# Kernel optimization log

Measured on AMD Instinct MI355X. Metric: run time of the kernel, lower is better.

Reference implementation:

```python
import jax, jax.numpy as jnp
import numpy as np

D_MODEL = 1024
N_HEAD = 16
D_HEAD = D_MODEL // N_HEAD
B, S = 4, 2048


def setup_inputs() -> dict:
    key = jax.random.key(0)
    ks = jax.random.split(key, 10)
    def xavier(k, shape):
        fan_in, fan_out = shape[1], shape[0]
        limit = np.sqrt(6.0 / (fan_in + fan_out))
        return jax.random.uniform(k, shape, jnp.float32, -limit, limit)
    x = jax.random.normal(ks[0], (B, S, D_MODEL), jnp.float32)
    mask = jnp.tril(jnp.ones((S, S), jnp.int32))[None, None]  # causal [1,1,S,S]
    return {
        "x": x,
        "Wq": xavier(ks[1], (D_MODEL, D_MODEL)), "bq": jnp.zeros((D_MODEL,), jnp.float32),
        "Wk": xavier(ks[2], (D_MODEL, D_MODEL)), "bk": jnp.zeros((D_MODEL,), jnp.float32),
        "Wv": xavier(ks[3], (D_MODEL, D_MODEL)), "bv": jnp.zeros((D_MODEL,), jnp.float32),
        "Wo": xavier(ks[4], (D_MODEL, D_MODEL)), "bo": jnp.zeros((D_MODEL,), jnp.float32),
        "mask": mask,
    }


def reference(x, Wq, bq, Wk, bk, Wv, bv, Wo, bo, mask):
    b, s, d = x.shape
    # Linear layers use y = x @ W.T + b (torch convention)
    def proj(W, bias):
        y = jnp.einsum('bsd,ed->bse', x, W) + bias
        return y.reshape(b, s, N_HEAD, D_HEAD).transpose(0, 2, 1, 3)  # [B,H,S,Dh]
    q = proj(Wq, bq)
    k = proj(Wk, bk)
    v = proj(Wv, bv)
    scores = jnp.einsum('bhqd,bhkd->bhqk', q, k) / jnp.sqrt(jnp.float32(D_HEAD))
    scores = jnp.where(mask == 0, jnp.float32(-1e9), scores)
    attn = jax.nn.softmax(scores, axis=-1)  # dropout is identity at eval
    context = jnp.einsum('bhqk,bhkd->bhqd', attn, v)
    context = context.transpose(0, 2, 1, 3).reshape(b, s, d)
    return jnp.einsum('bsd,ed->bse', context, Wo) + bo
```

## Files before the change

### kernel.cpp

```cpp
#include <hip/hip_runtime.h>
#include <stdint.h>

#define D_MODEL 1024
#define NHEAD   16
#define DHEAD   64
#define BATCH   4
#define SEQ     2048
#define MTOT    (BATCH*SEQ)

typedef __attribute__((ext_vector_type(4)))  float f32x4;
typedef __attribute__((ext_vector_type(8)))  short bf16x8;

typedef __attribute__((address_space(3))) uint32_t lds_u32;
typedef const __attribute__((address_space(1))) uint32_t glb_u32;

__device__ static inline void gload_lds16(const void* g, void* l) {
    __builtin_amdgcn_global_load_lds((glb_u32*)g, (lds_u32*)l, 16, 0, 0);
}

__device__ static inline ushort f2bf(float f) {
    uint32_t u = __builtin_bit_cast(uint32_t, f);
    u += 0x7fffu + ((u >> 16) & 1u);
    return (ushort)(u >> 16);
}

__device__ static inline float exp2_fast(float x) {
    float r; asm("v_exp_f32 %0, %1" : "=v"(r) : "v"(x)); return r;
}
__device__ static inline uint32_t cvt_pk_bf16(float a, float b) {
    uint32_t r;
    asm("v_cvt_pk_bf16_f32 %0, %1, %2" : "=v"(r) : "v"(a), "v"(b));
    return r;
}

__global__ __launch_bounds__(256) void convert_kernel(
    const float4* __restrict__ x,
    const float4* __restrict__ wq, const float4* __restrict__ wk,
    const float4* __restrict__ wv, const float4* __restrict__ wo,
    ushort4* __restrict__ xb, ushort4* __restrict__ wb)
{
    const int NX4 = (MTOT * D_MODEL) / 4;
    const int NW4 = (D_MODEL * D_MODEL) / 4;
    const int TOT = NX4 + 4 * NW4;
    for (int i = blockIdx.x * blockDim.x + threadIdx.x; i < TOT;
         i += gridDim.x * blockDim.x) {
        float4 v; ushort4* dst;
        if (i < NX4) { v = x[i]; dst = &xb[i]; }
        else {
            int j = i - NX4;
            int w = j >> 18;
            int r = j & (NW4 - 1);
            const float4* s = (w == 0) ? wq : (w == 1) ? wk : (w == 2) ? wv : wo;
            v = s[r]; dst = &wb[(size_t)w * NW4 + r];
        }
        ushort4 o;
        o.x = f2bf(v.x); o.y = f2bf(v.y); o.z = f2bf(v.z); o.w = f2bf(v.w);
        *dst = o;
    }
}


#define GEMM256_BODY(APTR, BPTR)                                            \
    __shared__ __align__(16) ushort S[2 * 32768];   \
    const int tid = threadIdx.x;                                            \
    const int w = tid >> 6, l = tid & 63;                                   \
    const int lo = l & 15, hi = l >> 4;                        \
    const int wm = w >> 2, wn = w & 3;                         \
    const int sr = l >> 3, sg = l & 7;                                      \
    f32x4 acc[8][4] = {};                                                   \
    auto stage = [&](int buf, int kt) {                                     \
        ushort* SP = &S[buf * 32768];                                       \
        _Pragma("unroll")                                                   \
        for (int j = 0; j < 4; ++j) {                                       \
            const int row = w * 32 + j * 8 + sr;                            \
            const int g = sg ^ sr;                         \
            gload_lds16((APTR) + (size_t)(m0 + row) * 1024 + kt * 64 + g * 8,\
                        SP + (w * 32 + j * 8) * 64);                        \
            gload_lds16((BPTR) + (size_t)(n0 + row) * 1024 + kt * 64 + g * 8,\
                        SP + 16384 + (w * 32 + j * 8) * 64);                \
        }                                                                   \
    };                                                                      \
    stage(0, 0);                                                            \
    asm volatile("s_waitcnt vmcnt(0)" ::: "memory");                        \
    __builtin_amdgcn_s_barrier();                                           \
    __builtin_amdgcn_sched_barrier(0);                                      \
    int cur = 0;                                                            \
    for (int kt = 0; kt < 16; ++kt) {                                       \
        if (kt + 1 < 16) stage(cur ^ 1, kt + 1);                            \
        const char* SA = (const char*)&S[cur * 32768];                      \
        const char* SB = SA + 32768;                                        \
        _Pragma("unroll")                                                   \
        for (int ks = 0; ks < 2; ++ks) {                                    \
            bf16x8 af[8], bfr[4];                                           \
            _Pragma("unroll")                                               \
            for (int mi = 0; mi < 8; ++mi) {                                \
                const int r = wm * 128 + mi * 16 + lo;                      \
                af[mi] = *(const bf16x8*)(SA + r * 128 +                    \
                          (((ks * 4 + hi) ^ (r & 7)) << 4));                \
            }                                                               \
            _Pragma("unroll")                                               \
            for (int ni = 0; ni < 4; ++ni) {                                \
                const int c = wn * 64 + ni * 16 + lo;                       \
                bfr[ni] = *(const bf16x8*)(SB + c * 128 +                   \
                          (((ks * 4 + hi) ^ (c & 7)) << 4));                \
            }                                                               \
            asm volatile("s_waitcnt lgkmcnt(0)" ::: "memory");              \
            __builtin_amdgcn_sched_barrier(0);                              \
            __builtin_amdgcn_s_setprio(1);                                  \
            _Pragma("unroll")                                               \
            for (int mi = 0; mi < 8; ++mi)                                  \
                _Pragma("unroll")                                           \
                for (int ni = 0; ni < 4; ++ni)                              \
                    acc[mi][ni] = __builtin_amdgcn_mfma_f32_16x16x32_bf16(  \
                        af[mi], bfr[ni], acc[mi][ni], 0, 0, 0);             \
            __builtin_amdgcn_s_setprio(0);                                  \
        }                                                                   \
        if (kt + 1 < 16) {                                                  \
            asm volatile("s_waitcnt vmcnt(0)" ::: "memory");                \
            __builtin_amdgcn_s_barrier();                                   \
            __builtin_amdgcn_sched_barrier(0);                              \
        }                                                                   \
        cur ^= 1;                                                           \
    }

__global__ __launch_bounds__(512) void gemm_qkv(
    const ushort* __restrict__ A,
    const ushort* __restrict__ W3,
    const float* __restrict__ bq, const float* __restrict__ bk,
    const float* __restrict__ bv,
    ushort* __restrict__ Qb, ushort* __restrict__ Kb, ushort* __restrict__ Vtb,
    float qscale)
{
    const int id = blockIdx.x;
    const int xcd = id & 7, q = id >> 3;
    const int mb = xcd * 4 + (q & 3);
    const int nb = q >> 2;
    const int m0 = mb * 256, n0 = nb * 256;

    GEMM256_BODY(A, W3)

    const int region = nb >> 2;
    const float scale = (region == 0) ? qscale : 1.0f;
    const float* bias = (region == 0) ? bq : (region == 1) ? bk : bv;
    ushort* outQK = (region == 0) ? Qb : Kb;

#pragma unroll
    for (int mi = 0; mi < 8; ++mi) {
#pragma unroll
        for (int ni = 0; ni < 4; ++ni) {
            const int gj  = n0 + wn * 64 + ni * 16 + lo;
            const int lcl = gj & 1023;
            const int h = lcl >> 6, dh = lcl & 63;
            const float bj = bias[lcl];
            const int gi0 = m0 + wm * 128 + mi * 16 + hi * 4;
            const int b = gi0 >> 11, s0 = gi0 & (SEQ - 1);
            if (region < 2) {
#pragma unroll
                for (int r = 0; r < 4; ++r)
                    outQK[(((size_t)(b * NHEAD + h)) * SEQ + s0 + r) * DHEAD + dh] =
                        f2bf((acc[mi][ni][r] + bj) * scale);
            } else {
                ushort4 o4;
                o4.x = f2bf(acc[mi][ni][0] + bj);
                o4.y = f2bf(acc[mi][ni][1] + bj);
                o4.z = f2bf(acc[mi][ni][2] + bj);
                o4.w = f2bf(acc[mi][ni][3] + bj);
                *(ushort4*)&Vtb[(((size_t)(b * NHEAD + h)) * DHEAD + dh) * SEQ + s0] = o4;
            }
        }
    }
}

__global__ __launch_bounds__(512) void gemm_out(
    const ushort* __restrict__ A,
    const ushort* __restrict__ W,
    const float*  __restrict__ bias,
    float* __restrict__ out)
{
    const int id = blockIdx.x;
    const int xcd = id & 7, q = id >> 3;
    const int mb = xcd * 4 + (q & 3);
    const int nb = q >> 2;
    const int m0 = mb * 256, n0 = nb * 256;

    GEMM256_BODY(A, W)

#pragma unroll
    for (int mi = 0; mi < 8; ++mi)
#pragma unroll
        for (int ni = 0; ni < 4; ++ni) {
            const int gj = n0 + wn * 64 + ni * 16 + lo;
            const float bj = bias[gj];
            const int gi0 = m0 + wm * 128 + mi * 16 + hi * 4;
#pragma unroll
            for (int r = 0; r < 4; ++r)
                out[(size_t)(gi0 + r) * D_MODEL + gj] = acc[mi][ni][r] + bj;
        }
}

__global__ __launch_bounds__(256) void attn_kernel(
    const ushort* __restrict__ Q, const ushort* __restrict__ K,
    const ushort* __restrict__ Vt, ushort* __restrict__ ctx)
{
    __shared__ __align__(16) ushort Ks[64 * 64];
    __shared__ __align__(16) ushort Vs[64 * 64];
    __shared__ __align__(16) ushort Pq[4 * 32 * 64];

    const int tid = threadIdx.x;
    const int w = tid >> 6, l = tid & 63, lo = l & 15, hi = l >> 4;
    const int sw = lo & 7;

    const int fid = blockIdx.x;
    const int xcd = fid & 7;
    const int u = fid >> 3;
    const int g = xcd * 8 + (u & 7);
    const int b = g >> 4, h = g & 15;
    const int j = u >> 3;
    const size_t base = (size_t)(b * NHEAD + h) * SEQ * DHEAD;

    const int krow = tid >> 3;
    const int kcol = (tid & 7) * 8;
    char* PqW = (char*)&Pq[w * 2048];

    for (int pass = 0; pass < 2; ++pass) {
        const int qt = pass ? (15 - j) : j;
        const int q0 = qt << 7;
        const int qw0 = q0 + w * 32;

        bf16x8 qf[2][2];
#pragma unroll
        for (int mi = 0; mi < 2; ++mi)
#pragma unroll
            for (int ks = 0; ks < 2; ++ks)
                qf[mi][ks] = *(const bf16x8*)&Q[base +
                    (size_t)(qw0 + mi * 16 + lo) * DHEAD + ks * 32 + hi * 8];

        f32x4 o[2][4] = {};
        float mrow[2] = {-1e30f, -1e30f}, lrow[2] = {0.f, 0.f};

        const int ntiles = (q0 + 128) >> 6;

        bf16x8 kregA[2], vregA[2], kregB[2], vregB[2];
#pragma unroll
        for (int c = 0; c < 2; ++c) {
            kregA[c] = *(const bf16x8*)&K[base + (size_t)(c * 32 + krow) * DHEAD + kcol];
            vregA[c] = *(const bf16x8*)&Vt[base + (size_t)(c * 32 + krow) * SEQ + kcol];
            kregB[c] = *(const bf16x8*)&K[base + (size_t)(64 + c * 32 + krow) * DHEAD + kcol];
            vregB[c] = *(const bf16x8*)&Vt[base + (size_t)(c * 32 + krow) * SEQ + 64 + kcol];
        }

        auto tile_body = [&](int t, bf16x8 (&KR)[2], bf16x8 (&VR)[2]) {
            const int kv0 = t << 6;
            __syncthreads();
#pragma unroll
            for (int c = 0; c < 2; ++c) {
                const int row = c * 32 + krow;
                const int g16 = (tid & 7) ^ (row & 7);
                *(bf16x8*)((char*)Ks + row * 128 + (g16 << 4)) = KR[c];
                *(bf16x8*)((char*)Vs + row * 128 + (g16 << 4)) = VR[c];
            }
            __syncthreads();
            if (t + 2 < ntiles) {
                const int nv0 = kv0 + 128;
#pragma unroll
                for (int c = 0; c < 2; ++c) {
                    KR[c] = *(const bf16x8*)&K[base + (size_t)(nv0 + c * 32 + krow) * DHEAD + kcol];
                    VR[c] = *(const bf16x8*)&Vt[base + (size_t)(c * 32 + krow) * SEQ + nv0 + kcol];
                }
            }
            if (kv0 > qw0 + 31) return;

            f32x4 s[2][4] = {};
            __builtin_amdgcn_s_setprio(1);
#pragma unroll
            for (int ks = 0; ks < 2; ++ks) {
                bf16x8 kf[4];
#pragma unroll
                for (int nj = 0; nj < 4; ++nj)
                    kf[nj] = *(const bf16x8*)((char*)Ks + (nj * 16 + lo) * 128 +
                                              ((((ks << 2) + hi) ^ sw) << 4));
#pragma unroll
                for (int mi = 0; mi < 2; ++mi)
#pragma unroll
                    for (int nj = 0; nj < 4; ++nj)
                        s[mi][nj] = __builtin_amdgcn_mfma_f32_16x16x32_bf16(
                            kf[nj], qf[mi][ks], s[mi][nj], 0, 0, 0);
            }
            __builtin_amdgcn_s_setprio(0);

            if (kv0 + 63 > qw0) {
#pragma unroll
                for (int mi = 0; mi < 2; ++mi) {
                    const int gq = qw0 + mi * 16 + lo;
#pragma unroll
                    for (int nj = 0; nj < 4; ++nj)
#pragma unroll
                        for (int r = 0; r < 4; ++r) {
                            const int gk = kv0 + nj * 16 + hi * 4 + r;
                            if (gk > gq) s[mi][nj][r] = -1e30f;
                        }
                }
            }

            float tl[2], corr[2];
#pragma unroll
            for (int mi = 0; mi < 2; ++mi) {
                float m = s[mi][0][0];
#pragma unroll
                for (int nj = 0; nj < 4; ++nj)
#pragma unroll
                    for (int r = 0; r < 4; ++r) m = fmaxf(m, s[mi][nj][r]);
                tl[mi] = m;
            }
            const bool grow = (tl[0] > mrow[0] + 8.f) | (tl[1] > mrow[1] + 8.f);
            if (__any(grow)) {
#pragma unroll
                for (int mi = 0; mi < 2; ++mi) {
                    float m2 = fmaxf(tl[mi], __shfl_xor(tl[mi], 16));
                    m2 = fmaxf(m2, __shfl_xor(m2, 32));
                    const float mn = fmaxf(mrow[mi], m2);
                    corr[mi] = exp2_fast(mrow[mi] - mn);
                    mrow[mi] = mn;
                }
#pragma unroll
                for (int mi = 0; mi < 2; ++mi)
#pragma unroll
                    for (int r = 0; r < 4; ++r) {
                        const float cb = __shfl(corr[mi], hi * 4 + r);
#pragma unroll
                        for (int ni = 0; ni < 4; ++ni) o[mi][ni][r] *= cb;
                    }
            } else { corr[0] = 1.f; corr[1] = 1.f; }

#pragma unroll
            for (int mi = 0; mi < 2; ++mi) {
                float ls = 0.f;
#pragma unroll
                for (int nj = 0; nj < 4; ++nj) {
#pragma unroll
                    for (int r = 0; r < 4; ++r) {
                        const float p = exp2_fast(s[mi][nj][r] - mrow[mi]);
                        s[mi][nj][r] = p;
                        ls += p;
                    }
                    uint2 pp;
                    pp.x = cvt_pk_bf16(s[mi][nj][0], s[mi][nj][1]);
                    pp.y = cvt_pk_bf16(s[mi][nj][2], s[mi][nj][3]);
                    const int gP = ((nj << 1) + (hi >> 1)) ^ sw;
                    *(uint2*)(PqW + (mi * 16 + lo) * 128 + (gP << 4) + ((hi & 1) << 3)) = pp;
                }
                ls += __shfl_xor(ls, 16);
                ls += __shfl_xor(ls, 32);
                lrow[mi] = lrow[mi] * corr[mi] + ls;
            }

            __builtin_amdgcn_s_setprio(1);
#pragma unroll
            for (int ks2 = 0; ks2 < 2; ++ks2) {
                bf16x8 pf[2], vf[4];
#pragma unroll
                for (int mi = 0; mi < 2; ++mi)
                    pf[mi] = *(const bf16x8*)(PqW + (mi * 16 + lo) * 128 +
                                              ((((ks2 << 2) + hi) ^ sw) << 4));
#pragma unroll
                for (int ni = 0; ni < 4; ++ni)
                    vf[ni] = *(const bf16x8*)((char*)Vs + (ni * 16 + lo) * 128 +
                                              ((((ks2 << 2) + hi) ^ sw) << 4));
#pragma unroll
                for (int mi = 0; mi < 2; ++mi)
#pragma unroll
                    for (int ni = 0; ni < 4; ++ni)
                        o[mi][ni] = __builtin_amdgcn_mfma_f32_16x16x32_bf16(
                            pf[mi], vf[ni], o[mi][ni], 0, 0, 0);
            }
            __builtin_amdgcn_s_setprio(0);
        };

        for (int tt = 0; tt < ntiles; tt += 2) {
            tile_body(tt,     kregA, vregA);
            tile_body(tt + 1, kregB, vregB);
        }

#pragma unroll
        for (int mi = 0; mi < 2; ++mi) {
            const float rv = 1.0f / lrow[mi];
#pragma unroll
            for (int r = 0; r < 4; ++r) {
                const float rb = __shfl(rv, hi * 4 + r);
                const int gq = qw0 + mi * 16 + hi * 4 + r;
#pragma unroll
                for (int ni = 0; ni < 4; ++ni)
                    ctx[((size_t)(b * SEQ + gq)) * D_MODEL + h * DHEAD + ni * 16 + lo] =
                        f2bf(o[mi][ni][r] * rb);
            }
        }
    }
}

extern "C" void kernel_launch(void* const* d_in, const int* in_sizes, int n_in,
                              void* d_out, int out_size, void* d_ws, size_t ws_size,
                              hipStream_t stream) {
    const float* x  = (const float*)d_in[0];
    const float* Wq = (const float*)d_in[1];
    const float* bq = (const float*)d_in[2];
    const float* Wk = (const float*)d_in[3];
    const float* bk = (const float*)d_in[4];
    const float* Wv = (const float*)d_in[5];
    const float* bv = (const float*)d_in[6];
    const float* Wo = (const float*)d_in[7];
    const float* bo = (const float*)d_in[8];

    char* ws = (char*)d_ws;
    ushort* xb  = (ushort*)(ws);
    ushort* wb  = (ushort*)(ws + (16u << 20));
    ushort* Qb  = (ushort*)(ws + (24u << 20));
    ushort* Kb  = (ushort*)(ws + (40u << 20));
    ushort* Vtb = (ushort*)(ws + (56u << 20));
    ushort* ctx = (ushort*)(ws + (72u << 20));

    convert_kernel<<<2048, 256, 0, stream>>>(
        (const float4*)x, (const float4*)Wq, (const float4*)Wk,
        (const float4*)Wv, (const float4*)Wo, (ushort4*)xb, (ushort4*)wb);

    const int NW = D_MODEL * D_MODEL;
    const float qscale = 0.125f * 1.44269504f;

    gemm_qkv<<<384, 512, 0, stream>>>(xb, wb, bq, bk, bv, Qb, Kb, Vtb, qscale);

    attn_kernel<<<512, 256, 0, stream>>>(Qb, Kb, Vtb, ctx);

    gemm_out<<<128, 512, 0, stream>>>(ctx, wb + 3 * NW, bo, (float*)d_out);
}
```

Before: 172.4 us.

## Load K and V fragments directly from global memory, dropping LDS staging

The attention kernel no longer stages K and V tiles into shared memory behind block-wide barriers with register double-buffering. Each wave now reads its MFMA fragments for K and Vt straight from global memory and loops only over the tiles its own 32 query rows need. This removes the two __syncthreads per tile and the LDS write/read traffic, and lets waves stop at their own causal bound. In exchange, the four waves re-fetch the same K/V data separately through L1/L2, and there is no explicit prefetch, so global load latency now sits directly in the compute loop.

Result: slower. 231.1 us (+34.1%).

```diff
diff --git a/kernel.cpp b/kernel.cpp
--- a/kernel.cpp
+++ b/kernel.cpp
@@ -202,8 +202,6 @@
     const ushort* __restrict__ Q, const ushort* __restrict__ K,
     const ushort* __restrict__ Vt, ushort* __restrict__ ctx)
 {
-    __shared__ __align__(16) ushort Ks[64 * 64];
-    __shared__ __align__(16) ushort Vs[64 * 64];
     __shared__ __align__(16) ushort Pq[4 * 32 * 64];
 
     const int tid = threadIdx.x;
@@ -218,8 +216,6 @@
     const int j = u >> 3;
     const size_t base = (size_t)(b * NHEAD + h) * SEQ * DHEAD;
 
-    const int krow = tid >> 3;
-    const int kcol = (tid & 7) * 8;
     char* PqW = (char*)&Pq[w * 2048];
 
     for (int pass = 0; pass < 2; ++pass) {
@@ -238,54 +234,29 @@
         f32x4 o[2][4] = {};
         float mrow[2] = {-1e30f, -1e30f}, lrow[2] = {0.f, 0.f};
 
-        const int ntiles = (q0 + 128) >> 6;
-
-        bf16x8 kregA[2], vregA[2], kregB[2], vregB[2];
-#pragma unroll
-        for (int c = 0; c < 2; ++c) {
-            kregA[c] = *(const bf16x8*)&K[base + (size_t)(c * 32 + krow) * DHEAD + kcol];
-            vregA[c] = *(const bf16x8*)&Vt[base + (size_t)(c * 32 + krow) * SEQ + kcol];
-            kregB[c] = *(const bf16x8*)&K[base + (size_t)(64 + c * 32 + krow) * DHEAD + kcol];
-            vregB[c] = *(const bf16x8*)&Vt[base + (size_t)(c * 32 + krow) * SEQ + 64 + kcol];
-        }
-
-        auto tile_body = [&](int t, bf16x8 (&KR)[2], bf16x8 (&VR)[2]) {
+        const int ntW = ((qw0 + 31) >> 6) + 1;
+
+        for (int t = 0; t < ntW; ++t) {
             const int kv0 = t << 6;
-            __syncthreads();
-#pragma unroll
-            for (int c = 0; c < 2; ++c) {
-                const int row = c * 32 + krow;
-                const int g16 = (tid & 7) ^ (row & 7);
-                *(bf16x8*)((char*)Ks + row * 128 + (g16 << 4)) = KR[c];
-                *(bf16x8*)((char*)Vs + row * 128 + (g16 << 4)) = VR[c];
-            }
-            __syncthreads();
-            if (t + 2 < ntiles) {
-                const int nv0 = kv0 + 128;
-#pragma unroll
-                for (int c = 0; c < 2; ++c) {
-                    KR[c] = *(const bf16x8*)&K[base + (size_t)(nv0 + c * 32 + krow) * DHEAD + kcol];
-                    VR[c] = *(const bf16x8*)&Vt[base + (size_t)(c * 32 + krow) * SEQ + nv0 + kcol];
-                }
-            }
-            if (kv0 > qw0 + 31) return;
+
+            bf16x8 kf[2][4];
+#pragma unroll
+            for (int ks = 0; ks < 2; ++ks)
+#pragma unroll
+                for (int nj = 0; nj < 4; ++nj)
+                    kf[ks][nj] = *(const bf16x8*)&K[base +
+                        (size_t)(kv0 + nj * 16 + lo) * DHEAD + ks * 32 + hi * 8];
 
             f32x4 s[2][4] = {};
             __builtin_amdgcn_s_setprio(1);
 #pragma unroll
-            for (int ks = 0; ks < 2; ++ks) {
-                bf16x8 kf[4];
-#pragma unroll
-                for (int nj = 0; nj < 4; ++nj)
-                    kf[nj] = *(const bf16x8*)((char*)Ks + (nj * 16 + lo) * 128 +
-                                              ((((ks << 2) + hi) ^ sw) << 4));
+            for (int ks = 0; ks < 2; ++ks)
 #pragma unroll
                 for (int mi = 0; mi < 2; ++mi)
 #pragma unroll
                     for (int nj = 0; nj < 4; ++nj)
                         s[mi][nj] = __builtin_amdgcn_mfma_f32_16x16x32_bf16(
-                            kf[nj], qf[mi][ks], s[mi][nj], 0, 0, 0);
-            }
+                            kf[ks][nj], qf[mi][ks], s[mi][nj], 0, 0, 0);
             __builtin_amdgcn_s_setprio(0);
 
             if (kv0 + 63 > qw0) {
@@ -359,14 +330,14 @@
             for (int ks2 = 0; ks2 < 2; ++ks2) {
                 bf16x8 pf[2], vf[4];
 #pragma unroll
+                for (int ni = 0; ni < 4; ++ni)
+                    vf[ni] = *(const bf16x8*)&Vt[base +
+                        (size_t)(ni * 16 + lo) * SEQ + kv0 + ks2 * 32 + hi * 8];
+#pragma unroll
                 for (int mi = 0; mi < 2; ++mi)
                     pf[mi] = *(const bf16x8*)(PqW + (mi * 16 + lo) * 128 +
                                               ((((ks2 << 2) + hi) ^ sw) << 4));
 #pragma unroll
-                for (int ni = 0; ni < 4; ++ni)
-                    vf[ni] = *(const bf16x8*)((char*)Vs + (ni * 16 + lo) * 128 +
-                                              ((((ks2 << 2) + hi) ^ sw) << 4));
-#pragma unroll
                 for (int mi = 0; mi < 2; ++mi)
 #pragma unroll
                     for (int ni = 0; ni < 4; ++ni)
@@ -374,11 +345,6 @@
                             pf[mi], vf[ni], o[mi][ni], 0, 0, 0);
             }
             __builtin_amdgcn_s_setprio(0);
-        };
-
-        for (int tt = 0; tt < ntiles; tt += 2) {
-            tile_body(tt,     kregA, vregA);
-            tile_body(tt + 1, kregB, vregB);
         }
 
 #pragma unroll
```
